# Kernel tuning notes

Hardware: AMD Instinct MI355X
Metric: run time of the kernel (lower is better)

Reference implementation:

```python
import jax, jax.numpy as jnp
import numpy as np

LATENT = 10
MAXLEN = 80
DT = 0.1
STEPS = int(round(1.0 / DT))
HIDDEN = 32
BATCH = 512


def _score_fn(xt_bld, time_b1, W1, b1, W2, b2):
    # score_model: flatten (B, L, D) -> concat time -> Dense(32, relu) -> Dense(D)
    B = xt_bld.shape[0]
    h = jnp.concatenate([xt_bld.reshape(B, -1), time_b1], axis=-1)  # (B, L*D+1)
    h = jax.nn.relu(h @ W1 + b1)
    return h @ W2 + b2  # (B, D)


def setup_inputs() -> dict:
    key = jax.random.key(0)
    k1, k2, k3, k4 = jax.random.split(key, 4)
    fan_in = MAXLEN * LATENT + 1  # 801
    z_mean = jax.random.normal(k1, (BATCH, MAXLEN, LATENT), jnp.float32)
    z_log_var = 0.1 * jax.random.normal(k2, (BATCH, MAXLEN, LATENT), jnp.float32)
    W1 = jax.random.normal(k3, (fan_in, HIDDEN), jnp.float32) / np.sqrt(fan_in)
    b1 = jnp.zeros((HIDDEN,), jnp.float32)
    W2 = jax.random.normal(k4, (HIDDEN, LATENT), jnp.float32) / np.sqrt(HIDDEN)
    b2 = jnp.zeros((LATENT,), jnp.float32)
    return {"z_mean": z_mean, "z_log_var": z_log_var, "W1": W1, "b1": b1, "W2": W2, "b2": b2}


def _diffusion_loss(z_mean, z_log_var, W1, b1, W2, b2):
    B = z_mean.shape[0]
    sigma = jnp.exp(z_log_var)                    # ez_log_var in train_step
    mu_tr = jnp.transpose(z_mean, (1, 0, 2))      # (L, B, D)
    sigma_tr = jnp.transpose(sigma, (1, 0, 2))    # (L, B, D)
    zero = jnp.zeros((1, B, LATENT), mu_tr.dtype)
    full_mu_ext = jnp.concatenate([zero, mu_tr], axis=0)       # (L+1, B, D)
    full_sigma_ext = jnp.concatenate([zero, sigma_tr], axis=0)  # (L+1, B, D)
    noise_keys = jax.random.split(jax.random.key(1337), MAXLEN * (STEPS + 1)).reshape(MAXLEN, STEPS + 1)

    def diffusion_step(i, mu_i, sigma_i, keys):
        # mask_below_target_step: keep rows < i
        mask = (jnp.arange(MAXLEN) < i).astype(mu_tr.dtype)[:, None, None]
        masked_mu = mu_tr * mask                                   # (L, B, D)
        times = i.astype(jnp.float32) + jnp.arange(STEPS, dtype=jnp.float32) * DT
        sigma_std = jnp.sqrt(sigma_i)                              # (B, D)
        x0 = mu_i + sigma_std * jax.random.normal(keys[0], (B, LATENT))

        def body(xt, xs):
            t, k = xs
            t_idx = jnp.floor(t).astype(jnp.int32)
            next_mu = jax.lax.dynamic_index_in_dim(full_mu_ext, t_idx + 1, 0, keepdims=False)
            next_sigma = jax.lax.dynamic_index_in_dim(full_sigma_ext, t_idx + 1, 0, keepdims=False)
            one_hot = jax.nn.one_hot(t_idx, MAXLEN, dtype=xt.dtype)     # (L,)
            score_in = masked_mu + one_hot[:, None, None] * xt[None]    # (L, B, D)
            score_in = jnp.transpose(score_in, (1, 0, 2))               # (B, L, D)
            time_col = jnp.full((B, 1), t, xt.dtype)
            score = _score_fn(score_in, time_col, W1, b1, W2, b2)       # (B, D)
            logdx = -(xt - next_mu) / jnp.sqrt(next_sigma)
            err = jnp.abs(logdx - score)
            dW = jax.random.normal(k, (B, LATENT)) * jnp.sqrt(DT)
            xt = xt + 0.5 * jnp.square(sigma_std) * score + sigma_std * dW
            return xt, err

        xt_final, errs = jax.lax.scan(body, x0, (times, keys[1:]))
        return xt_final, errs.sum(axis=0)  # tf.reduce_sum(error, axis=0)

    seq, err = jax.vmap(diffusion_step)(jnp.arange(MAXLEN), mu_tr, sigma_tr, noise_keys)
    sequence = jnp.transpose(seq, (1, 0, 2))       # (B, L, D)
    score_error = jnp.transpose(err, (1, 0, 2))    # (B, L, D)
    return sequence, score_error


def reference(z_mean, z_log_var, W1, b1, W2, b2):
    return _diffusion_loss(z_mean, z_log_var, W1, b1, W2, b2)
```

## Files before the change

### kernel.cpp

```cpp
#include <hip/hip_runtime.h>
#include <stdint.h>

#define LATENT 10
#define MAXLEN 80
#define STEPS  10
#define HIDDEN 32
#define BATCH  512
#define NSEG   16
#define SEGL   5

__device__ __forceinline__ void tf2x32(uint32_t k0, uint32_t k1,
                                       uint32_t x0, uint32_t x1,
                                       uint32_t& o0, uint32_t& o1) {
  uint32_t ks2 = k0 ^ k1 ^ 0x1BD11BDAu;
  uint32_t v0 = x0 + k0;
  uint32_t v1 = x1 + k1;
#define TF_R(rot) { v0 += v1; v1 = (v1 << (rot)) | (v1 >> (32 - (rot))); v1 ^= v0; }
  TF_R(13) TF_R(15) TF_R(26) TF_R(6)
  v0 += k1;  v1 += ks2 + 1u;
  TF_R(17) TF_R(29) TF_R(16) TF_R(24)
  v0 += ks2; v1 += k0 + 2u;
  TF_R(13) TF_R(15) TF_R(26) TF_R(6)
  v0 += k0;  v1 += k1 + 3u;
  TF_R(17) TF_R(29) TF_R(16) TF_R(24)
  v0 += k1;  v1 += ks2 + 4u;
  TF_R(13) TF_R(15) TF_R(26) TF_R(6)
  v0 += ks2; v1 += k0 + 5u;
#undef TF_R
  o0 = v0; o1 = v1;
}

__device__ __forceinline__ float bits_to_normal(uint32_t bits) {
  const float lo = -0.99999994f;
  float f = __uint_as_float((bits >> 9) | 0x3f800000u) - 1.0f;
  float u = fmaf(f, 2.0f, lo);
  u = fmaxf(u, lo);
  float w = -log1pf(-u * u);
  float p;
  if (w < 5.0f) {
    w -= 2.5f;
    p = 2.81022636e-08f;
    p = fmaf(p, w, 3.43273939e-07f);
    p = fmaf(p, w, -3.5233877e-06f);
    p = fmaf(p, w, -4.39150654e-06f);
    p = fmaf(p, w, 0.00021858087f);
    p = fmaf(p, w, -0.00125372503f);
    p = fmaf(p, w, -0.00417768164f);
    p = fmaf(p, w, 0.246640727f);
    p = fmaf(p, w, 1.50140941f);
  } else {
    w = sqrtf(w) - 3.0f;
    p = -0.000200214257f;
    p = fmaf(p, w, 0.000100950558f);
    p = fmaf(p, w, 0.00134934322f);
    p = fmaf(p, w, -0.00367342844f);
    p = fmaf(p, w, 0.00573950773f);
    p = fmaf(p, w, -0.0076224613f);
    p = fmaf(p, w, 0.00943887047f);
    p = fmaf(p, w, 1.00167406f);
    p = fmaf(p, w, 2.83297682f);
  }
  return 1.4142135623730951f * (p * u);
}

__global__ __launch_bounds__(256) void k_seg(
    const float* __restrict__ zmean, const float* __restrict__ W1,
    float* __restrict__ segtot) {
  int id = blockIdx.x * 256 + threadIdx.x;
  int s = id >> 14;
  int r = id & 16383;
  int b = r >> 5, j = r & 31;
  float pf0 = 0.0f, pf1 = 0.0f;
#pragma unroll
  for (int t = 0; t < SEGL; ++t) {
    int l = s * SEGL + t;
    const float2* mrow = (const float2*)(zmean + (b * MAXLEN + l) * LATENT);
    float2 m0 = mrow[0], m1 = mrow[1], m2 = mrow[2], m3 = mrow[3], m4 = mrow[4];
    const float* wl = W1 + (l * LATENT) * HIDDEN + j;
    pf0 = fmaf(m0.x, wl[0 * HIDDEN], pf0);
    pf1 = fmaf(m0.y, wl[1 * HIDDEN], pf1);
    pf0 = fmaf(m1.x, wl[2 * HIDDEN], pf0);
    pf1 = fmaf(m1.y, wl[3 * HIDDEN], pf1);
    pf0 = fmaf(m2.x, wl[4 * HIDDEN], pf0);
    pf1 = fmaf(m2.y, wl[5 * HIDDEN], pf1);
    pf0 = fmaf(m3.x, wl[6 * HIDDEN], pf0);
    pf1 = fmaf(m3.y, wl[7 * HIDDEN], pf1);
    pf0 = fmaf(m4.x, wl[8 * HIDDEN], pf0);
    pf1 = fmaf(m4.y, wl[9 * HIDDEN], pf1);
  }
  segtot[(s * BATCH + b) * HIDDEN + j] = pf0 + pf1;
}

__global__ __launch_bounds__(256) void k_chain(
    const float* __restrict__ zmean, const float* __restrict__ zlv,
    const float* __restrict__ W1, const float* __restrict__ b1v,
    const float* __restrict__ W2, const float* __restrict__ b2v,
    const float* __restrict__ segtot,
    float* __restrict__ outSeq, float* __restrict__ outErr) {
  __shared__ float nrmS[(STEPS + 1) * LATENT * 32];
  __shared__ uint32_t skk[2 * (STEPS + 1)];

  const int tid = threadIdx.x;
  const int i = blockIdx.x >> 4;
  const int b0 = (blockIdx.x & 15) << 5;

  if (tid < (STEPS + 1)) {
    uint32_t a, c;
    tf2x32(0u, 1337u, 0u, (uint32_t)(i * (STEPS + 1) + tid), a, c);
    skk[2 * tid] = a; skk[2 * tid + 1] = c;
  }
  __syncthreads();

  for (int rr = 0; rr < 14; ++rr) {
    int idx = rr * 256 + tid;
    if (idx < 3520) {
      int c = idx & 31, n = idx >> 5;
      int k = (n * 205) >> 11;
      int d = n - k * 10;
      uint32_t o0, o1;
      tf2x32(skk[2 * k], skk[2 * k + 1], 0u,
             (uint32_t)((b0 + c) * LATENT + d), o0, o1);
      nrmS[n * 32 + c] = bits_to_normal(o0 ^ o1);
    }
  }
  __syncthreads();

  const int r = tid & 7;
  const int jb = r * 4;
  const int cloc = tid >> 3;
  const int b = b0 + cloc;

  const float* rowT = W1 + (MAXLEN * LATENT) * HIDDEN;
  float pf[4], wT[4];
  const float fi = (float)i;
#pragma unroll
  for (int k = 0; k < 4; ++k) {
    wT[k] = rowT[jb + k];
    pf[k] = fmaf(fi, wT[k], b1v[jb + k]);
  }
  const int fs = i / SEGL;
  for (int s2 = 0; s2 < fs; ++s2) {
    float4 t0 = *(const float4*)(segtot + ((size_t)s2 * BATCH + b) * HIDDEN + jb);
    pf[0] += t0.x; pf[1] += t0.y; pf[2] += t0.z; pf[3] += t0.w;
  }
  for (int l = fs * SEGL; l < i; ++l) {
    const float2* mrow = (const float2*)(zmean + (b * MAXLEN + l) * LATENT);
    const float* wl = W1 + (l * LATENT) * HIDDEN + jb;
#pragma unroll
    for (int p = 0; p < 5; ++p) {
      float2 m = mrow[p];
      float4 wa = *(const float4*)(wl + (2 * p) * HIDDEN);
      float4 wb = *(const float4*)(wl + (2 * p + 1) * HIDDEN);
      pf[0] = fmaf(m.x, wa.x, pf[0]); pf[1] = fmaf(m.x, wa.y, pf[1]);
      pf[2] = fmaf(m.x, wa.z, pf[2]); pf[3] = fmaf(m.x, wa.w, pf[3]);
      pf[0] = fmaf(m.y, wb.x, pf[0]); pf[1] = fmaf(m.y, wb.y, pf[1]);
      pf[2] = fmaf(m.y, wb.z, pf[2]); pf[3] = fmaf(m.y, wb.w, pf[3]);
    }
  }

  const int base = (b * MAXLEN + i) * LATENT;
  float mu[LATENT], sstd[LATENT], u[LATENT], errs[LATENT], b2[LATENT];
  {
    const float2* zm = (const float2*)(zmean + base);
    const float2* zl = (const float2*)(zlv + base);
#pragma unroll
    for (int p = 0; p < 5; ++p) {
      float2 m = zm[p], v = zl[p];
      mu[2 * p] = m.x; mu[2 * p + 1] = m.y;
      sstd[2 * p] = sqrtf(expf(v.x));
      sstd[2 * p + 1] = sqrtf(expf(v.y));
    }
  }
#pragma unroll
  for (int d = 0; d < LATENT; ++d) {
    b2[d] = b2v[d];
    errs[d] = 0.0f;
    u[d] = nrmS[d * 32 + cloc];
  }

  const float* W1i = W1 + (i * LATENT) * HIDDEN + jb;
  const float* W2q = W2 + jb * LATENT;
  const float SQRT_DT = 0.31622776601683794f;

  for (int s = 0; s < STEPS; ++s) {
    float nd[LATENT];
#pragma unroll
    for (int d = 0; d < LATENT; ++d)
      nd[d] = nrmS[((s + 1) * LATENT + d) * 32 + cloc];

    float xt[LATENT];
#pragma unroll
    for (int d = 0; d < LATENT; ++d) xt[d] = fmaf(sstd[d], u[d], mu[d]);

    const float ts = (float)s * 0.1f;
    float h[4];
#pragma unroll
    for (int k = 0; k < 4; ++k) h[k] = fmaf(ts, wT[k], pf[k]);
#pragma unroll
    for (int d = 0; d < LATENT; ++d) {
      const float xd = xt[d];
      float4 w = *(const float4*)(W1i + d * HIDDEN);
      h[0] = fmaf(xd, w.x, h[0]); h[1] = fmaf(xd, w.y, h[1]);
      h[2] = fmaf(xd, w.z, h[2]); h[3] = fmaf(xd, w.w, h[3]);
    }
    float sc[LATENT];
#pragma unroll
    for (int d = 0; d < LATENT; ++d) sc[d] = 0.0f;
#pragma unroll
    for (int k = 0; k < 4; ++k) {
      const float hj = fmaxf(h[k], 0.0f);
      const float2* w2r = (const float2*)(W2q + k * LATENT);
#pragma unroll
      for (int p = 0; p < 5; ++p) {
        float2 w = w2r[p];
        sc[2 * p] = fmaf(hj, w.x, sc[2 * p]);
        sc[2 * p + 1] = fmaf(hj, w.y, sc[2 * p + 1]);
      }
    }
#pragma unroll
    for (int m = 1; m < 8; m <<= 1) {
#pragma unroll
      for (int d = 0; d < LATENT; ++d) sc[d] += __shfl_xor(sc[d], m);
    }
#pragma unroll
    for (int d = 0; d < LATENT; ++d) {
      float st = sc[d] + b2[d];
      errs[d] += fabsf(u[d] + st);
      float ndw = nd[d] * SQRT_DT;
      u[d] = u[d] + fmaf(0.5f * sstd[d], st, ndw);
    }
  }

#pragma unroll
  for (int d = 0; d < LATENT; ++d) {
    if ((d & 7) == r) {
      outSeq[base + d] = fmaf(sstd[d], u[d], mu[d]);
      outErr[base + d] = errs[d];
    }
  }
}

__global__ __launch_bounds__(64) void k_mono(
    const float* __restrict__ zmean, const float* __restrict__ zlv,
    const float* __restrict__ W1, const float* __restrict__ b1v,
    const float* __restrict__ W2, const float* __restrict__ b2v,
    float* __restrict__ outSeq, float* __restrict__ outErr) {
  int i = blockIdx.x >> 3;
  int b = ((blockIdx.x & 7) << 6) + threadIdx.x;
  float pref[HIDDEN];
#pragma unroll
  for (int j = 0; j < HIDDEN; ++j) pref[j] = 0.0f;
  for (int l = 0; l < i; ++l) {
    const float* mrow = zmean + (b * MAXLEN + l) * LATENT;
    const float* wrow = W1 + (l * LATENT) * HIDDEN;
#pragma unroll
    for (int d = 0; d < LATENT; ++d) {
      float m = mrow[d];
#pragma unroll
      for (int j = 0; j < HIDDEN; ++j) pref[j] = fmaf(m, wrow[d * HIDDEN + j], pref[j]);
    }
  }
  const int base = (b * MAXLEN + i) * LATENT;
  float mu[LATENT], sstd[LATENT], xt[LATENT], errs[LATENT];
#pragma unroll
  for (int d = 0; d < LATENT; ++d) {
    mu[d] = zmean[base + d];
    sstd[d] = sqrtf(expf(zlv[base + d]));
  }
  float n0[LATENT];
  {
    uint32_t a, c;
    tf2x32(0u, 1337u, 0u, (uint32_t)(i * (STEPS + 1)), a, c);
#pragma unroll
    for (int d = 0; d < LATENT; ++d) {
      uint32_t o0, o1;
      tf2x32(a, c, 0u, (uint32_t)(b * LATENT + d), o0, o1);
      n0[d] = bits_to_normal(o0 ^ o1);
    }
  }
#pragma unroll
  for (int d = 0; d < LATENT; ++d) { xt[d] = mu[d] + sstd[d] * n0[d]; errs[d] = 0.0f; }
  const float* rowT  = W1 + (MAXLEN * LATENT) * HIDDEN;
  const float* rowsI = W1 + (i * LATENT) * HIDDEN;
  const float SQRT_DT = 0.31622776601683794f;
  for (int s = 0; s < STEPS; ++s) {
    float t = (float)i + (float)s * 0.1f;
    float h[HIDDEN];
#pragma unroll
    for (int j = 0; j < HIDDEN; ++j) h[j] = pref[j];
#pragma unroll
    for (int d = 0; d < LATENT; ++d) {
      float xd = xt[d];
      const float* row = rowsI + d * HIDDEN;
#pragma unroll
      for (int j = 0; j < HIDDEN; ++j) h[j] = fmaf(xd, row[j], h[j]);
    }
    float sc[LATENT];
#pragma unroll
    for (int d = 0; d < LATENT; ++d) sc[d] = b2v[d];
#pragma unroll
    for (int j = 0; j < HIDDEN; ++j) {
      float hj = fmaf(t, rowT[j], h[j]) + b1v[j];
      hj = fmaxf(hj, 0.0f);
      const float* w2r = W2 + j * LATENT;
#pragma unroll
      for (int d = 0; d < LATENT; ++d) sc[d] = fmaf(hj, w2r[d], sc[d]);
    }
    float nd[LATENT];
    {
      uint32_t a, c;
      tf2x32(0u, 1337u, 0u, (uint32_t)(i * (STEPS + 1) + s + 1), a, c);
#pragma unroll
      for (int d = 0; d < LATENT; ++d) {
        uint32_t o0, o1;
        tf2x32(a, c, 0u, (uint32_t)(b * LATENT + d), o0, o1);
        nd[d] = bits_to_normal(o0 ^ o1);
      }
    }
#pragma unroll
    for (int d = 0; d < LATENT; ++d) {
      float logdx = -(xt[d] - mu[d]) / sstd[d];
      errs[d] += fabsf(logdx - sc[d]);
      float dW = nd[d] * SQRT_DT;
      xt[d] = xt[d] + (0.5f * (sstd[d] * sstd[d])) * sc[d] + sstd[d] * dW;
    }
  }
#pragma unroll
  for (int d = 0; d < LATENT; ++d) {
    outSeq[base + d] = xt[d];
    outErr[base + d] = errs[d];
  }
}

extern "C" void kernel_launch(void* const* d_in, const int* in_sizes, int n_in,
                              void* d_out, int out_size, void* d_ws, size_t ws_size,
                              hipStream_t stream) {
  (void)in_sizes; (void)n_in; (void)out_size;
  const float* zmean = (const float*)d_in[0];
  const float* zlv   = (const float*)d_in[1];
  const float* W1    = (const float*)d_in[2];
  const float* b1v   = (const float*)d_in[3];
  const float* W2    = (const float*)d_in[4];
  const float* b2v   = (const float*)d_in[5];
  float* outSeq = (float*)d_out;
  float* outErr = outSeq + (size_t)BATCH * MAXLEN * LATENT;

  const size_t segBytes = (size_t)NSEG * BATCH * HIDDEN * sizeof(float);

  if (ws_size >= segBytes) {
    float* segtot = (float*)d_ws;
    hipLaunchKernelGGL(k_seg, dim3(NSEG * BATCH * HIDDEN / 256), dim3(256), 0, stream,
                       zmean, W1, segtot);
    hipLaunchKernelGGL(k_chain, dim3(MAXLEN * 16), dim3(256), 0, stream,
                       zmean, zlv, W1, b1v, W2, b2v, segtot, outSeq, outErr);
  } else {
    hipLaunchKernelGGL(k_mono, dim3(MAXLEN * 8), dim3(64), 0, stream,
                       zmean, zlv, W1, b1v, W2, b2v, outSeq, outErr);
  }
}
```

Baseline: 124.1 us.

## Halve batch columns per block and fold sigma and mu into precomputed W1 terms

The chain kernel now handles 16 batch columns per block instead of 32 and launches twice as many blocks, so the normal-noise generation work per block is halved. Only 128 of the 256 threads continue into the recurrence after the noise is generated. The mu·W1 term is folded into the per-thread prefix and sigma is pre-multiplied into the per-step W1 weights, so each step works directly on u and no longer builds xt or reloads W1. SQRT_DT is folded into the stored noise, and log1pf is replaced with the fast __logf(1-u²), which may slightly change precision for the noise draws.

```diff
diff --git a/kernel.cpp b/kernel.cpp
--- a/kernel.cpp
+++ b/kernel.cpp
@@ -8,6 +8,7 @@
 #define BATCH  512
 #define NSEG   16
 #define SEGL   5
+#define CPB    16
 
 __device__ __forceinline__ void tf2x32(uint32_t k0, uint32_t k1,
                                        uint32_t x0, uint32_t x1,
@@ -35,7 +36,7 @@
   float f = __uint_as_float((bits >> 9) | 0x3f800000u) - 1.0f;
   float u = fmaf(f, 2.0f, lo);
   u = fmaxf(u, lo);
-  float w = -log1pf(-u * u);
+  float w = -__logf(fmaf(-u, u, 1.0f));
   float p;
   if (w < 5.0f) {
     w -= 2.5f;
@@ -97,12 +98,12 @@
     const float* __restrict__ W2, const float* __restrict__ b2v,
     const float* __restrict__ segtot,
     float* __restrict__ outSeq, float* __restrict__ outErr) {
-  __shared__ float nrmS[(STEPS + 1) * LATENT * 32];
+  __shared__ float nrmS[(STEPS + 1) * LATENT * CPB];
   __shared__ uint32_t skk[2 * (STEPS + 1)];
 
   const int tid = threadIdx.x;
-  const int i = blockIdx.x >> 4;
-  const int b0 = (blockIdx.x & 15) << 5;
+  const int i = blockIdx.x >> 5;
+  const int b0 = (blockIdx.x & 31) << 4;
 
   if (tid < (STEPS + 1)) {
     uint32_t a, c;
@@ -111,20 +112,24 @@
   }
   __syncthreads();
 
-  for (int rr = 0; rr < 14; ++rr) {
+  const float SQRT_DT = 0.31622776601683794f;
+#pragma unroll
+  for (int rr = 0; rr < 7; ++rr) {
     int idx = rr * 256 + tid;
-    if (idx < 3520) {
-      int c = idx & 31, n = idx >> 5;
+    if (idx < (STEPS + 1) * LATENT * CPB) {
+      int c = idx & (CPB - 1), n = idx >> 4;
       int k = (n * 205) >> 11;
       int d = n - k * 10;
       uint32_t o0, o1;
       tf2x32(skk[2 * k], skk[2 * k + 1], 0u,
              (uint32_t)((b0 + c) * LATENT + d), o0, o1);
-      nrmS[n * 32 + c] = bits_to_normal(o0 ^ o1);
+      float v = bits_to_normal(o0 ^ o1);
+      nrmS[n * CPB + c] = (n < LATENT) ? v : v * SQRT_DT;
     }
   }
   __syncthreads();
 
+  if (tid >= 8 * CPB) return;
   const int r = tid & 7;
   const int jb = r * 4;
   const int cloc = tid >> 3;
@@ -159,38 +164,45 @@
   }
 
   const int base = (b * MAXLEN + i) * LATENT;
-  float mu[LATENT], sstd[LATENT], u[LATENT], errs[LATENT], b2[LATENT];
+  float mu[LATENT], shalf[LATENT], u[LATENT], errs[LATENT], b2[LATENT];
+  float w1s[LATENT][4];
   {
     const float2* zm = (const float2*)(zmean + base);
     const float2* zl = (const float2*)(zlv + base);
+    const float* W1i = W1 + (i * LATENT) * HIDDEN + jb;
 #pragma unroll
     for (int p = 0; p < 5; ++p) {
       float2 m = zm[p], v = zl[p];
+      float s0 = sqrtf(expf(v.x));
+      float s1 = sqrtf(expf(v.y));
       mu[2 * p] = m.x; mu[2 * p + 1] = m.y;
-      sstd[2 * p] = sqrtf(expf(v.x));
-      sstd[2 * p + 1] = sqrtf(expf(v.y));
+      shalf[2 * p] = 0.5f * s0; shalf[2 * p + 1] = 0.5f * s1;
+      float4 wa = *(const float4*)(W1i + (2 * p) * HIDDEN);
+      float4 wb = *(const float4*)(W1i + (2 * p + 1) * HIDDEN);
+      pf[0] = fmaf(m.x, wa.x, pf[0]); pf[1] = fmaf(m.x, wa.y, pf[1]);
+      pf[2] = fmaf(m.x, wa.z, pf[2]); pf[3] = fmaf(m.x, wa.w, pf[3]);
+      pf[0] = fmaf(m.y, wb.x, pf[0]); pf[1] = fmaf(m.y, wb.y, pf[1]);
+      pf[2] = fmaf(m.y, wb.z, pf[2]); pf[3] = fmaf(m.y, wb.w, pf[3]);
+      w1s[2 * p][0] = s0 * wa.x; w1s[2 * p][1] = s0 * wa.y;
+      w1s[2 * p][2] = s0 * wa.z; w1s[2 * p][3] = s0 * wa.w;
+      w1s[2 * p + 1][0] = s1 * wb.x; w1s[2 * p + 1][1] = s1 * wb.y;
+      w1s[2 * p + 1][2] = s1 * wb.z; w1s[2 * p + 1][3] = s1 * wb.w;
     }
   }
 #pragma unroll
   for (int d = 0; d < LATENT; ++d) {
     b2[d] = b2v[d];
     errs[d] = 0.0f;
-    u[d] = nrmS[d * 32 + cloc];
-  }
-
-  const float* W1i = W1 + (i * LATENT) * HIDDEN + jb;
+    u[d] = nrmS[d * CPB + cloc];
+  }
+
   const float* W2q = W2 + jb * LATENT;
-  const float SQRT_DT = 0.31622776601683794f;
 
   for (int s = 0; s < STEPS; ++s) {
     float nd[LATENT];
 #pragma unroll
     for (int d = 0; d < LATENT; ++d)
-      nd[d] = nrmS[((s + 1) * LATENT + d) * 32 + cloc];
-
-    float xt[LATENT];
-#pragma unroll
-    for (int d = 0; d < LATENT; ++d) xt[d] = fmaf(sstd[d], u[d], mu[d]);
+      nd[d] = nrmS[((s + 1) * LATENT + d) * CPB + cloc];
 
     const float ts = (float)s * 0.1f;
     float h[4];
@@ -198,10 +210,9 @@
     for (int k = 0; k < 4; ++k) h[k] = fmaf(ts, wT[k], pf[k]);
 #pragma unroll
     for (int d = 0; d < LATENT; ++d) {
-      const float xd = xt[d];
-      float4 w = *(const float4*)(W1i + d * HIDDEN);
-      h[0] = fmaf(xd, w.x, h[0]); h[1] = fmaf(xd, w.y, h[1]);
-      h[2] = fmaf(xd, w.z, h[2]); h[3] = fmaf(xd, w.w, h[3]);
+      const float ud = u[d];
+      h[0] = fmaf(ud, w1s[d][0], h[0]); h[1] = fmaf(ud, w1s[d][1], h[1]);
+      h[2] = fmaf(ud, w1s[d][2], h[2]); h[3] = fmaf(ud, w1s[d][3], h[3]);
     }
     float sc[LATENT];
 #pragma unroll
@@ -226,15 +237,15 @@
     for (int d = 0; d < LATENT; ++d) {
       float st = sc[d] + b2[d];
       errs[d] += fabsf(u[d] + st);
-      float ndw = nd[d] * SQRT_DT;
-      u[d] = u[d] + fmaf(0.5f * sstd[d], st, ndw);
+      u[d] = u[d] + fmaf(shalf[d], st, nd[d]);
     }
   }
 
 #pragma unroll
   for (int d = 0; d < LATENT; ++d) {
     if ((d & 7) == r) {
-      outSeq[base + d] = fmaf(sstd[d], u[d], mu[d]);
+      float sd = shalf[d] + shalf[d];
+      outSeq[base + d] = fmaf(sd, u[d], mu[d]);
       outErr[base + d] = errs[d];
     }
   }
@@ -351,7 +362,7 @@
     float* segtot = (float*)d_ws;
     hipLaunchKernelGGL(k_seg, dim3(NSEG * BATCH * HIDDEN / 256), dim3(256), 0, stream,
                        zmean, W1, segtot);
-    hipLaunchKernelGGL(k_chain, dim3(MAXLEN * 16), dim3(256), 0, stream,
+    hipLaunchKernelGGL(k_chain, dim3(MAXLEN * (BATCH / CPB)), dim3(256), 0, stream,
                        zmean, zlv, W1, b1v, W2, b2v, segtot, outSeq, outErr);
   } else {
     hipLaunchKernelGGL(k_mono, dim3(MAXLEN * 8), dim3(64), 0, stream,
```

New measurement: 113.2 us. -8.7%, faster.
